# Kernel optimization log

Measured on AMD Instinct MI355X. Metric: run time of the kernel, lower is better.

## Reference

```python
import jax, jax.numpy as jnp
import numpy as np

N = 20000       # nodes
E = 160000      # edges (avg degree 8)
NFEAT = 512
NHID = 512
NCLASS = 64
NLAYERS = 4


def setup_inputs() -> dict:
    key = jax.random.key(0)
    ks = jax.random.split(key, 9)
    s = 0.05
    x = jax.random.normal(ks[0], (N, NFEAT), dtype=jnp.float32)
    edge_index = jax.random.randint(ks[1], (2, E), 0, N, dtype=jnp.int64)
    W_enc = jax.random.normal(ks[2], (NFEAT, NHID), dtype=jnp.float32) * s
    b_enc = jnp.zeros((NHID,), dtype=jnp.float32)
    W_convs = jax.random.normal(ks[3], (NLAYERS, NHID, NHID), dtype=jnp.float32) * s
    b_convs = jnp.zeros((NLAYERS, NHID), dtype=jnp.float32)
    W_dec = jax.random.normal(ks[4], (NHID, NCLASS), dtype=jnp.float32) * s
    b_dec = jnp.zeros((NCLASS,), dtype=jnp.float32)
    return {"x": x, "edge_index": edge_index, "W_enc": W_enc, "b_enc": b_enc,
            "W_convs": W_convs, "b_convs": b_convs, "W_dec": W_dec, "b_dec": b_dec}


def reference(x, edge_index, W_enc, b_enc, W_convs, b_convs, W_dec, b_dec):
    n = x.shape[0]
    loops = jnp.arange(n, dtype=edge_index.dtype)
    # GCNConv adds self-loops, then sym-normalizes: D^-1/2 (A+I) D^-1/2
    src = jnp.concatenate([edge_index[0], loops])  # [E+N]
    dst = jnp.concatenate([edge_index[1], loops])  # [E+N]
    deg = jax.ops.segment_sum(jnp.ones_like(dst, dtype=x.dtype), dst, num_segments=N)
    dinv = jnp.where(deg > 0, jax.lax.rsqrt(deg), jnp.zeros_like(deg))
    norm = (dinv[src] * dinv[dst])[:, None]  # [E+N, 1]

    # encoder: relu(Linear)
    h = jax.nn.relu(x @ W_enc + b_enc)

    def gcn_step(h, wb):
        W, b = wb
        hW = h @ W                                   # [N, H]
        msg = hW[src] * norm                         # gather + scale
        agg = jax.ops.segment_sum(msg, dst, num_segments=N)  # scatter-add
        return jax.nn.relu(agg + b), None            # bias after aggregation (PyG)

    h, _ = jax.lax.scan(gcn_step, h, (W_convs, b_convs))

    # decoder (dropout p=0 in eval -> identity)
    return h @ W_dec + b_dec
```

## Files before the change

kernel.cpp:

```cpp
#include <hip/hip_runtime.h>

#define N_NODES 20000
#define E_EDGES 160000
#define NFEAT   512
#define NHID    512
#define NCLASS  64
#define NLAYERS 4

#define SCAN_CHUNK 1024
#define NBLK ((N_NODES + SCAN_CHUNK - 1) / SCAN_CHUNK)
#define CNT_BLOCKS ((E_EDGES + 255) / 256)
#define CVT_BLOCKS ((N_NODES * NFEAT) / 2048)

using bf16x8 = __attribute__((ext_vector_type(8))) short;
using f32x4  = __attribute__((ext_vector_type(4))) float;
using u16x8  = __attribute__((ext_vector_type(8))) unsigned short;

__device__ __forceinline__ unsigned short f2bf(float f) {
    union { float f; unsigned int u; } v; v.f = f;
    unsigned int u = v.u + 0x7FFFu + ((v.u >> 16) & 1u);
    return (unsigned short)(u >> 16);
}
__device__ __forceinline__ float bf2f(unsigned short h) {
    union { unsigned int u; float f; } v; v.u = ((unsigned int)h) << 16;
    return v.f;
}
__device__ __forceinline__ void gl2lds16(const void* gptr, void* lptr) {
    __builtin_amdgcn_global_load_lds(
        (const __attribute__((address_space(1))) unsigned int*)gptr,
        (__attribute__((address_space(3))) unsigned int*)lptr,
        16, 0, 0);
}

__global__ __launch_bounds__(256) void prep_all(const int* __restrict__ dst,
                                                int* __restrict__ counts,
                                                int* __restrict__ bsums,
                                                const float* __restrict__ W_enc,
                                                const float* __restrict__ W_convs,
                                                const float* __restrict__ W_dec,
                                                unsigned short* __restrict__ WencT,
                                                unsigned short* __restrict__ WcvT,
                                                unsigned short* __restrict__ WdecT,
                                                const float* __restrict__ x,
                                                unsigned short* __restrict__ Xbf) {
    __shared__ int bins[NBLK];
    __shared__ float tile[32][33];
    const int b = blockIdx.x, t = threadIdx.x;

    if (b < CNT_BLOCKS) {
        if (t < NBLK) bins[t] = 0;
        __syncthreads();
        const int e = b * 256 + t;
        if (e < E_EDGES) {
            const int d = dst[e];
            atomicAdd(&counts[d], 1);
            atomicAdd(&bins[d >> 10], 1);
        }
        __syncthreads();
        if (t < NBLK && bins[t]) atomicAdd(&bsums[t], bins[t]);
        return;
    }

    if (b >= CNT_BLOCKS + 6 * 256) {
        const int cid = b - CNT_BLOCKS - 6 * 256;
        const size_t base = (size_t)cid * 2048 + (size_t)t * 8;
        const float4 f0 = *(const float4*)(x + base);
        const float4 f1 = *(const float4*)(x + base + 4);
        u16x8 pk;
        pk[0] = f2bf(f0.x); pk[1] = f2bf(f0.y);
        pk[2] = f2bf(f0.z); pk[3] = f2bf(f0.w);
        pk[4] = f2bf(f1.x); pk[5] = f2bf(f1.y);
        pk[6] = f2bf(f1.z); pk[7] = f2bf(f1.w);
        *(u16x8*)(Xbf + base) = pk;
        return;
    }

    const int bid = b - CNT_BLOCKS;
    const int id  = bid >> 8;
    const int rem = bid & 255;
    const int n0  = (rem & 15) * 32;
    const int k0  = (rem >> 4) * 32;
    const float* W; unsigned short* WT; int N;
    const int K = 512;
    if (id == 0)            { W = W_enc; WT = WencT; N = NHID; }
    else if (id <= NLAYERS) { W = W_convs + (size_t)(id - 1) * NHID * NHID;
                              WT = WcvT  + (size_t)(id - 1) * NHID * NHID; N = NHID; }
    else                    { W = W_dec; WT = WdecT; N = NCLASS; }
    if (n0 >= N) return;
    const int tx = t & 31, ty = t >> 5;
#pragma unroll
    for (int i = 0; i < 32; i += 8)
        tile[ty + i][tx] = W[(size_t)(k0 + ty + i) * N + n0 + tx];
    __syncthreads();
#pragma unroll
    for (int i = 0; i < 32; i += 8)
        WT[(size_t)(n0 + ty + i) * K + k0 + tx] = f2bf(tile[tx][ty + i]);
}

__global__ __launch_bounds__(256) void write_rowptr(const int* __restrict__ counts,
                                                    const int* __restrict__ bsums,
                                                    int* __restrict__ row_ptr,
                                                    int* __restrict__ cursor,
                                                    float* __restrict__ dinv) {
    __shared__ int part[256];
    __shared__ int boff_s;
    const int b = blockIdx.x, t = threadIdx.x;

    if (t < 64) {
        int v = (t < NBLK && t < b) ? bsums[t] : 0;
        for (int off = 32; off > 0; off >>= 1) v += __shfl_xor(v, off, 64);
        if (t == 0) boff_s = v;
    }

    const int base = b * SCAN_CHUNK + t * 4;
    int c[4], s = 0;
    for (int i = 0; i < 4; ++i) {
        int idx = base + i;
        c[i] = (idx < N_NODES) ? counts[idx] : 0;
        s += c[i];
    }
    part[t] = s;
    __syncthreads();
    for (int off = 1; off < 256; off <<= 1) {
        int v = (t >= off) ? part[t - off] : 0;
        __syncthreads();
        part[t] += v;
        __syncthreads();
    }
    int run = boff_s + ((t == 0) ? 0 : part[t - 1]);
    for (int i = 0; i < 4; ++i) {
        int idx = base + i;
        if (idx < N_NODES) {
            row_ptr[idx] = run;
            cursor[idx]  = run;
            dinv[idx]    = rsqrtf((float)c[i] + 1.0f);
            run += c[i];
        }
    }
    if (b == 0 && t == 0) row_ptr[N_NODES] = E_EDGES;
}

__global__ __launch_bounds__(256) void csr_fill(const int* __restrict__ src,
                                                const int* __restrict__ dst,
                                                const float* __restrict__ dinv,
                                                int* __restrict__ cursor,
                                                int2* __restrict__ ew) {
    int e = blockIdx.x * 256 + threadIdx.x;
    if (e < E_EDGES) {
        int s = src[e], d = dst[e];
        int pos = atomicAdd(&cursor[d], 1);
        ew[pos] = make_int2(s, __float_as_int(dinv[s] * dinv[d]));
    }
    if (e < 8) ew[E_EDGES + e] = make_int2(0, 0);
}

template <int R, int BN, bool RELU, bool HASBIAS, bool OUTBF16>
__global__ __launch_bounds__(256) void gemm_bres(const unsigned short* __restrict__ A,
                                                 const unsigned short* __restrict__ BT,
                                                 const float* __restrict__ bias,
                                                 void* __restrict__ Cout,
                                                 int M, int N) {
    constexpr int K  = 512;
    constexpr int BM = 4 * R * 16;
    constexpr int C  = BN / 16;
    __shared__ unsigned short lB[BN * K];

    const int t    = threadIdx.x;
    const int lane = t & 63;
    const int wv   = t >> 6;
    const int lm   = lane & 15;
    const int q    = lane >> 4;

    const int MBLK = (M + BM - 1) / BM;
    const int NBN  = N / BN;
    int mblk, nblk;
    {
        const int i    = blockIdx.x;
        const int full = (MBLK / 8) * 8 * NBN;
        if (i < full) {
            const int g = i / (8 * NBN);
            const int l = i % (8 * NBN);
            mblk = g * 8 + (l & 7);
            nblk = l >> 3;
        } else {
            const int t2  = i - full;
            const int rem = MBLK & 7;
            mblk = (MBLK / 8) * 8 + t2 % rem;
            nblk = t2 / rem;
        }
    }
    const int m0 = mblk * BM;
    const int n0 = nblk * BN;

#pragma unroll
    for (int i = 0; i < (BN * 64) / 256; ++i) {
        const int idx = i * 256 + t;
        const int row = idx >> 6;
        const int c64 = idx & 63;
        const int g   = (c64 & ~7) | ((c64 & 7) ^ (row & 7));
        gl2lds16(BT + (size_t)(n0 + row) * K + g * 8, &lB[idx * 8]);
    }
    __syncthreads();

    const unsigned short* ap[R];
#pragma unroll
    for (int r = 0; r < R; ++r) {
        int gr = m0 + wv * R * 16 + r * 16 + lm;
        if (gr >= M) gr = M - 1;
        ap[r] = A + (size_t)gr * K + q * 8;
    }

    f32x4 acc[R][C] = {};
    bf16x8 aC[R], aN[R];
#pragma unroll
    for (int r = 0; r < R; ++r) aC[r] = *(const bf16x8*)ap[r];

    for (int kt = 0; kt < K; kt += 32) {
        if (kt + 32 < K) {
#pragma unroll
            for (int r = 0; r < R; ++r)
                aN[r] = *(const bf16x8*)(ap[r] + kt + 32);
        }
        bf16x8 bf[C];
        const int cb = kt >> 3;
#pragma unroll
        for (int c = 0; c < C; ++c) {
            const int row  = c * 16 + lm;
            const int c64  = cb + q;
            const int phys = (c64 & ~7) | ((c64 & 7) ^ (row & 7));
            bf[c] = *(const bf16x8*)&lB[row * K + phys * 8];
        }
#pragma unroll
        for (int r = 0; r < R; ++r)
#pragma unroll
            for (int c = 0; c < C; ++c)
                acc[r][c] = __builtin_amdgcn_mfma_f32_16x16x32_bf16(
                    aC[r], bf[c], acc[r][c], 0, 0, 0);
#pragma unroll
        for (int r = 0; r < R; ++r) aC[r] = aN[r];
    }

#pragma unroll
    for (int r = 0; r < R; ++r) {
#pragma unroll
        for (int c = 0; c < C; ++c) {
            const int colg = n0 + c * 16 + lm;
            const float bb = HASBIAS ? bias[colg] : 0.0f;
            const int rowb = m0 + wv * R * 16 + r * 16 + q * 4;
#pragma unroll
            for (int i = 0; i < 4; ++i) {
                const int rr = rowb + i;
                if (rr < M) {
                    float v = acc[r][c][i] + bb;
                    if (RELU) v = fmaxf(v, 0.0f);
                    if (OUTBF16)
                        ((unsigned short*)Cout)[(size_t)rr * N + colg] = f2bf(v);
                    else
                        ((float*)Cout)[(size_t)rr * N + colg] = v;
                }
            }
        }
    }
}

__global__ __launch_bounds__(256) void gcn_aggregate(const unsigned short* __restrict__ hW,
                                                     const int* __restrict__ row_ptr,
                                                     const int2* __restrict__ ew,
                                                     const float* __restrict__ dinv,
                                                     const float* __restrict__ bias,
                                                     unsigned short* __restrict__ out) {
    const int wv   = threadIdx.x >> 6;
    const int lane = threadIdx.x & 63;
    int d = blockIdx.x * 4 + wv;
    d = __builtin_amdgcn_readfirstlane(d);
    if (d >= N_NODES) return;
    const int beg = __builtin_amdgcn_readfirstlane(row_ptr[d]);
    const int end = __builtin_amdgcn_readfirstlane(row_ptr[d + 1]);
    const size_t foff = (size_t)lane * 8;

    const float di = dinv[d];
    const float sl = di * di;
    u16x8 sv = *(const u16x8*)(hW + (size_t)d * NHID + foff);
    float acc[8];
#pragma unroll
    for (int i = 0; i < 8; ++i) acc[i] = bf2f(sv[i]) * sl;

    for (int j = beg; j < end; j += 8) {
        int   sK[8];
        float wK[8];
        u16x8 v[8];
#pragma unroll
        for (int k = 0; k < 8; ++k) {
            const int jj = j + k;
            const int2 e = ew[jj];
            const bool valid = jj < end;
            sK[k] = valid ? e.x : 0;
            wK[k] = valid ? __int_as_float(e.y) : 0.0f;
        }
#pragma unroll
        for (int k = 0; k < 8; ++k)
            v[k] = *(const u16x8*)(hW + (size_t)sK[k] * NHID + foff);
#pragma unroll
        for (int k = 0; k < 8; ++k)
#pragma unroll
            for (int i = 0; i < 8; ++i)
                acc[i] += bf2f(v[k][i]) * wK[k];
    }

    const float4 b0v = *(const float4*)(bias + foff);
    const float4 b1v = *(const float4*)(bias + foff + 4);
    u16x8 r;
    r[0] = f2bf(fmaxf(acc[0] + b0v.x, 0.0f));
    r[1] = f2bf(fmaxf(acc[1] + b0v.y, 0.0f));
    r[2] = f2bf(fmaxf(acc[2] + b0v.z, 0.0f));
    r[3] = f2bf(fmaxf(acc[3] + b0v.w, 0.0f));
    r[4] = f2bf(fmaxf(acc[4] + b1v.x, 0.0f));
    r[5] = f2bf(fmaxf(acc[5] + b1v.y, 0.0f));
    r[6] = f2bf(fmaxf(acc[6] + b1v.z, 0.0f));
    r[7] = f2bf(fmaxf(acc[7] + b1v.w, 0.0f));
    *(u16x8*)(out + (size_t)d * NHID + foff) = r;
}

extern "C" void kernel_launch(void* const* d_in, const int* in_sizes, int n_in,
                              void* d_out, int out_size, void* d_ws, size_t ws_size,
                              hipStream_t stream) {
    const float* x       = (const float*)d_in[0];
    const int*   ei      = (const int*)d_in[1];
    const float* W_enc   = (const float*)d_in[2];
    const float* b_enc   = (const float*)d_in[3];
    const float* W_convs = (const float*)d_in[4];
    const float* b_convs = (const float*)d_in[5];
    const float* W_dec   = (const float*)d_in[6];
    const float* b_dec   = (const float*)d_in[7];
    float* out = (float*)d_out;

    const int* src = ei;
    const int* dst = ei + E_EDGES;

    char* ws = (char*)d_ws;
    auto alloc = [&](size_t bytes) {
        char* p = ws;
        ws += (bytes + 255) / 256 * 256;
        return p;
    };
    float* dinv     = (float*)alloc(N_NODES * 4);
    int*   counts   = (int*)  alloc((N_NODES + NBLK) * 4);
    int*   bsums    = counts + N_NODES;
    int*   row_ptr  = (int*)  alloc((N_NODES + 1) * 4);
    int*   cursor   = (int*)  alloc(N_NODES * 4);
    int2*  ew       = (int2*) alloc((E_EDGES + 8) * 8);
    unsigned short* WencT = (unsigned short*)alloc((size_t)NFEAT * NHID * 2);
    unsigned short* WcvT  = (unsigned short*)alloc((size_t)NLAYERS * NHID * NHID * 2);
    unsigned short* WdecT = (unsigned short*)alloc((size_t)NHID * NCLASS * 2);
    unsigned short* B1    = (unsigned short*)alloc((size_t)N_NODES * NHID * 2);
    unsigned short* B2    = (unsigned short*)alloc((size_t)N_NODES * NHID * 2);
    unsigned short* Xbf   = B2;

    hipMemsetAsync(counts, 0, (N_NODES + NBLK) * sizeof(int), stream);
    prep_all<<<CNT_BLOCKS + 6 * 256 + CVT_BLOCKS, 256, 0, stream>>>(
        dst, counts, bsums, W_enc, W_convs, W_dec, WencT, WcvT, WdecT, x, Xbf);
    write_rowptr<<<NBLK, 256, 0, stream>>>(counts, bsums, row_ptr, cursor, dinv);
    csr_fill<<<(E_EDGES + 255) / 256, 256, 0, stream>>>(src, dst, dinv, cursor, ew);

    const int MBLK256 = (N_NODES + 255) / 256;
    const int MBLK128 = (N_NODES + 127) / 128;

    gemm_bres<4, 64, true, true, true>
        <<<MBLK256 * (NHID / 64), 256, 0, stream>>>(
        Xbf, WencT, b_enc, B1, N_NODES, NHID);

    for (int L = 0; L < NLAYERS; ++L) {
        gemm_bres<4, 64, false, false, true>
            <<<MBLK256 * (NHID / 64), 256, 0, stream>>>(
            B1, WcvT + (size_t)L * NHID * NHID, nullptr, B2, N_NODES, NHID);
        gcn_aggregate<<<(N_NODES + 3) / 4, 256, 0, stream>>>(
            B2, row_ptr, ew, dinv, b_convs + (size_t)L * NHID, B1);
    }

    gemm_bres<2, 64, false, true, false>
        <<<MBLK128 * (NCLASS / 64), 256, 0, stream>>>(
        B1, WdecT, b_dec, out, N_NODES, NCLASS);
}
```

Before: 407.8 us.

## Split GEMM weight staging into two K halves and shrink row tile for occupancy

```diff
diff --git a/kernel.cpp b/kernel.cpp
--- a/kernel.cpp
+++ b/kernel.cpp
@@ -154,16 +154,18 @@
     if (e < 8) ew[E_EDGES + e] = make_int2(0, 0);
 }
 
-template <int R, int BN, bool RELU, bool HASBIAS, bool OUTBF16>
-__global__ __launch_bounds__(256) void gemm_bres(const unsigned short* __restrict__ A,
-                                                 const unsigned short* __restrict__ BT,
-                                                 const float* __restrict__ bias,
-                                                 void* __restrict__ Cout,
-                                                 int M, int N) {
+template <int R, bool RELU, bool HASBIAS, bool OUTBF16>
+__global__ __launch_bounds__(256, 5) void gemm_bres(const unsigned short* __restrict__ A,
+                                                    const unsigned short* __restrict__ BT,
+                                                    const float* __restrict__ bias,
+                                                    void* __restrict__ Cout,
+                                                    int M, int N) {
     constexpr int K  = 512;
+    constexpr int KH = 256;
+    constexpr int BN = 64;
     constexpr int BM = 4 * R * 16;
     constexpr int C  = BN / 16;
-    __shared__ unsigned short lB[BN * K];
+    __shared__ unsigned short lB[BN * KH];
 
     const int t    = threadIdx.x;
     const int lane = t & 63;
@@ -192,16 +194,6 @@
     const int m0 = mblk * BM;
     const int n0 = nblk * BN;
 
-#pragma unroll
-    for (int i = 0; i < (BN * 64) / 256; ++i) {
-        const int idx = i * 256 + t;
-        const int row = idx >> 6;
-        const int c64 = idx & 63;
-        const int g   = (c64 & ~7) | ((c64 & 7) ^ (row & 7));
-        gl2lds16(BT + (size_t)(n0 + row) * K + g * 8, &lB[idx * 8]);
-    }
-    __syncthreads();
-
     const unsigned short* ap[R];
 #pragma unroll
     for (int r = 0; r < R; ++r) {
@@ -215,29 +207,44 @@
 #pragma unroll
     for (int r = 0; r < R; ++r) aC[r] = *(const bf16x8*)ap[r];
 
-    for (int kt = 0; kt < K; kt += 32) {
-        if (kt + 32 < K) {
+    for (int half = 0; half < 2; ++half) {
+        if (half) __syncthreads();
+        const int kh = half * KH;
+#pragma unroll
+        for (int i = 0; i < (BN * (KH / 8)) / 256; ++i) {
+            const int idx = i * 256 + t;
+            const int row = idx >> 5;
+            const int c32 = idx & 31;
+            const int g   = (c32 & ~7) | ((c32 & 7) ^ (row & 7));
+            gl2lds16(BT + (size_t)(n0 + row) * K + kh + g * 8, &lB[idx * 8]);
+        }
+        __syncthreads();
+
+#pragma unroll
+        for (int s = 0; s < 8; ++s) {
+            const int ks = half * 8 + s;
+            if (ks < 15) {
+#pragma unroll
+                for (int r = 0; r < R; ++r)
+                    aN[r] = *(const bf16x8*)(ap[r] + (ks + 1) * 32);
+            }
+            bf16x8 bf[C];
+#pragma unroll
+            for (int c = 0; c < C; ++c) {
+                const int row  = c * 16 + lm;
+                const int c32  = s * 4 + q;
+                const int phys = (c32 & ~7) | ((c32 & 7) ^ (row & 7));
+                bf[c] = *(const bf16x8*)&lB[row * KH + phys * 8];
+            }
 #pragma unroll
             for (int r = 0; r < R; ++r)
-                aN[r] = *(const bf16x8*)(ap[r] + kt + 32);
-        }
-        bf16x8 bf[C];
-        const int cb = kt >> 3;
-#pragma unroll
-        for (int c = 0; c < C; ++c) {
-            const int row  = c * 16 + lm;
-            const int c64  = cb + q;
-            const int phys = (c64 & ~7) | ((c64 & 7) ^ (row & 7));
-            bf[c] = *(const bf16x8*)&lB[row * K + phys * 8];
-        }
-#pragma unroll
-        for (int r = 0; r < R; ++r)
-#pragma unroll
-            for (int c = 0; c < C; ++c)
-                acc[r][c] = __builtin_amdgcn_mfma_f32_16x16x32_bf16(
-                    aC[r], bf[c], acc[r][c], 0, 0, 0);
-#pragma unroll
-        for (int r = 0; r < R; ++r) aC[r] = aN[r];
+#pragma unroll
+                for (int c = 0; c < C; ++c)
+                    acc[r][c] = __builtin_amdgcn_mfma_f32_16x16x32_bf16(
+                        aC[r], bf[c], acc[r][c], 0, 0, 0);
+#pragma unroll
+            for (int r = 0; r < R; ++r) aC[r] = aN[r];
+        }
     }
 
 #pragma unroll
@@ -362,22 +369,21 @@
     write_rowptr<<<NBLK, 256, 0, stream>>>(counts, bsums, row_ptr, cursor, dinv);
     csr_fill<<<(E_EDGES + 255) / 256, 256, 0, stream>>>(src, dst, dinv, cursor, ew);
 
-    const int MBLK256 = (N_NODES + 255) / 256;
     const int MBLK128 = (N_NODES + 127) / 128;
 
-    gemm_bres<4, 64, true, true, true>
-        <<<MBLK256 * (NHID / 64), 256, 0, stream>>>(
+    gemm_bres<2, true, true, true>
+        <<<MBLK128 * (NHID / 64), 256, 0, stream>>>(
         Xbf, WencT, b_enc, B1, N_NODES, NHID);
 
     for (int L = 0; L < NLAYERS; ++L) {
-        gemm_bres<4, 64, false, false, true>
-            <<<MBLK256 * (NHID / 64), 256, 0, stream>>>(
+        gemm_bres<2, false, false, true>
+            <<<MBLK128 * (NHID / 64), 256, 0, stream>>>(
             B1, WcvT + (size_t)L * NHID * NHID, nullptr, B2, N_NODES, NHID);
         gcn_aggregate<<<(N_NODES + 3) / 4, 256, 0, stream>>>(
             B2, row_ptr, ew, dinv, b_convs + (size_t)L * NHID, B1);
     }
 
-    gemm_bres<2, 64, false, true, false>
+    gemm_bres<2, false, true, false>
         <<<MBLK128 * (NCLASS / 64), 256, 0, stream>>>(
         B1, WdecT, b_dec, out, N_NODES, NCLASS);
 }
```

New measurement: 397.8 us. -2.5%, faster.
